# Kernel tuning notes

Measured on AMD Instinct MI355X. Metric: run time of the kernel, lower is better.

The kernel has to match this reference:

```python
import jax, jax.numpy as jnp
import numpy as np

H, D = 20, 64  # heads, head_dim (hidden_size = 1280)


def setup_inputs() -> dict:
    key = jax.random.key(0)
    ks = jax.random.split(key, 10)
    B, S, HID, CROSS, T_TXT, T_IP = 8, 4096, 1280, 2048, 77, 4
    w = lambda k, shp: jax.random.normal(k, shp, dtype=jnp.float32) * 0.02
    return {
        "hidden_states": jax.random.normal(ks[0], (B, S, HID), dtype=jnp.float32),
        "encoder_hidden_states": jax.random.normal(ks[1], (B, T_TXT, CROSS), dtype=jnp.float32),
        "ip_hidden_states": jax.random.normal(ks[2], (B, T_IP, CROSS), dtype=jnp.float32),
        "Wq": w(ks[3], (HID, HID)),
        "Wk": w(ks[4], (CROSS, HID)),
        "Wv": w(ks[5], (CROSS, HID)),
        "Wk_ip": w(ks[6], (CROSS, HID)),
        "Wv_ip": w(ks[7], (CROSS, HID)),
        "Wo": w(ks[8], (HID, HID)),
        "bo": jnp.zeros((HID,), dtype=jnp.float32),
    }


def _attend(q, kv_in, Wk, Wv):
    # q: [B,S,H,D]; kv_in: [B,T,cross]
    B, T = kv_in.shape[0], kv_in.shape[1]
    k = (kv_in @ Wk).reshape(B, T, H, D)
    v = (kv_in @ Wv).reshape(B, T, H, D)
    scale = 1.0 / jnp.sqrt(jnp.asarray(D, q.dtype))
    scores = jnp.einsum("bqhd,bkhd->bhqk", q, k) * scale
    probs = jax.nn.softmax(scores, axis=-1)
    out = jnp.einsum("bhqk,bkhd->bqhd", probs, v)
    return out.reshape(B, q.shape[1], H * D)


def reference(hidden_states, encoder_hidden_states, ip_hidden_states,
              Wq, Wk, Wv, Wk_ip, Wv_ip, Wo, bo):
    B, S, _ = hidden_states.shape
    q = (hidden_states @ Wq).reshape(B, S, H, D)
    # text cross-attention branch
    out = _attend(q, encoder_hidden_states, Wk, Wv)
    # IP-adapter branch (single adapter, scale=1.0, no mask)
    ip_scale = 1.0
    out = out + ip_scale * _attend(q, ip_hidden_states, Wk_ip, Wv_ip)
    # output projection (dropout is identity at inference)
    return out @ Wo + bo
```

## Files before the change

kernel.cpp:

```cpp
#include <hip/hip_runtime.h>

using u16 = unsigned short;
using u32 = unsigned int;
typedef __bf16 bf16x8 __attribute__((ext_vector_type(8)));
typedef float f32x4 __attribute__((ext_vector_type(4)));
typedef float f32x16 __attribute__((ext_vector_type(16)));

__device__ __forceinline__ u16 f2bf(float f) {
  u32 u = __float_as_uint(f);
  u += 0x7FFFu + ((u >> 16) & 1u);
  return (u16)(u >> 16);
}

__device__ __forceinline__ u32 cvtpk(float a, float b) {
  u32 r;
  asm("v_cvt_pk_bf16_f32 %0, %1, %2" : "=v"(r) : "v"(a), "v"(b));
  return r;
}

__device__ __forceinline__ void gload16(const u16* g, u16* l) {
  __builtin_amdgcn_global_load_lds((const __attribute__((address_space(1))) void*)g,
                                   (__attribute__((address_space(3))) void*)l, 16, 0, 0);
}

__global__ void build_a_all(const float* __restrict__ enc, const float* __restrict__ ip,
                            u16* __restrict__ out) {
  const int i = blockIdx.x * 256 + threadIdx.x;
  const int row = i >> 9;
  const int c4 = i & 511;
  ushort4 o = {0, 0, 0, 0};
  const float4* src = nullptr;
  if (row < 616) src = (const float4*)enc + (size_t)row * 512 + c4;
  else if (row >= 640 && row < 672) src = (const float4*)ip + (size_t)(row - 640) * 512 + c4;
  if (src) {
    const float4 v = *src;
    o.x = f2bf(v.x); o.y = f2bf(v.y); o.z = f2bf(v.z); o.w = f2bf(v.w);
  }
  ((ushort4*)out)[i] = o;
}

__global__ void transpose_w4(const float* __restrict__ s0, const float* __restrict__ s1,
                             const float* __restrict__ s2, const float* __restrict__ s3,
                             u16* __restrict__ dst) {
  __shared__ float tile[32][33];
  const int z = blockIdx.z;
  const float* in = (z == 0) ? s0 : (z == 1) ? s1 : (z == 2) ? s2 : s3;
  u16* out = dst + (size_t)z * 1280 * 2048;
  const int K = 2048, N = 1280;
  const int n0 = blockIdx.x << 5, k0 = blockIdx.y << 5;
  const int x = threadIdx.x, y = threadIdx.y;
#pragma unroll
  for (int i = 0; i < 32; i += 8)
    tile[y + i][x] = in[(size_t)(k0 + y + i) * N + n0 + x];
  __syncthreads();
#pragma unroll
  for (int i = 0; i < 32; i += 8)
    out[(size_t)(n0 + y + i) * K + k0 + x] = f2bf(tile[x][y + i]);
}

__global__ void transpose_w2(const float* __restrict__ s0, const float* __restrict__ s1,
                             u16* __restrict__ d0, u16* __restrict__ d1) {
  __shared__ float tile[32][33];
  const int z = blockIdx.z;
  const float* in = z ? s1 : s0;
  u16* out = z ? d1 : d0;
  const int K = 1280, N = 1280;
  const int n0 = blockIdx.x << 5, k0 = blockIdx.y << 5;
  const int x = threadIdx.x, y = threadIdx.y;
#pragma unroll
  for (int i = 0; i < 32; i += 8)
    tile[y + i][x] = in[(size_t)(k0 + y + i) * N + n0 + x];
  __syncthreads();
#pragma unroll
  for (int i = 0; i < 32; i += 8)
    out[(size_t)(n0 + y + i) * K + k0 + x] = f2bf(tile[x][y + i]);
}

#define MFMA16(a, b, c) __builtin_amdgcn_mfma_f32_16x16x32_bf16(a, b, c, 0, 0, 0)
#define MFMA32(a, b, c) __builtin_amdgcn_mfma_f32_32x32x16_bf16(a, b, c, 0, 0, 0)

template <int MODE, int CONV>
__global__ __launch_bounds__(512, 2) void gemm256(
    const u16* __restrict__ A, const u16* __restrict__ Bt,
    u16* __restrict__ Cb, float* __restrict__ Cf, const float* __restrict__ bias,
    const u16* __restrict__ kvcP, const u16* __restrict__ vtP,
    const float* __restrict__ convSrc, u16* __restrict__ convDst,
    int M, int N, int K) {
  const int tid = threadIdx.x;

  if (CONV) {
    if (blockIdx.x >= 60) {
      const float4* src = (const float4*)convSrc;
      ushort4* dst = (ushort4*)convDst;
      const long base = (long)(blockIdx.x - 60) * 4096 + tid;
#pragma unroll
      for (int k = 0; k < 8; ++k) {
        const float4 v = src[base + k * 512];
        ushort4 o;
        o.x = f2bf(v.x); o.y = f2bf(v.y); o.z = f2bf(v.z); o.w = f2bf(v.w);
        dst[base + k * 512] = o;
      }
      return;
    }
  }

  __shared__ __align__(16) u16 smem[67584];
  u16* As = smem;
  u16* Bs = smem + 32768;

  const int w = tid >> 6, lane = tid & 63;
  const int lo = lane & 15, hi = lane >> 4;
  const int wm = w >> 2, wn = w & 3;

  const int nbn = N >> 8;
  int wg = blockIdx.x;
  if (!CONV) {
    const int nwg = gridDim.x;
    const int q = nwg >> 3, r = nwg & 7;
    const int xcd = wg & 7, l = wg >> 3;
    wg = (xcd < r ? xcd * (q + 1) : r * (q + 1) + (xcd - r) * q) + l;
  }
  const int bm = wg / nbn, bn = wg % nbn;
  const int m0 = bm << 8, n0 = bn << 8;
  const int NT = K >> 6;

  const int sr = lane >> 3;
  const int sc8 = ((lane & 7) ^ sr) << 3;
  const u16* pA[2];
  const u16* pB[2];
#pragma unroll
  for (int i = 0; i < 2; ++i) {
    const int rr = (i * 8 + w) * 8 + sr;
    pA[i] = A + (size_t)(m0 + rr) * K + sc8;
    pB[i] = Bt + (size_t)(n0 + rr) * K + sc8;
  }
  const int ch0 = w * 512, ch1 = (8 + w) * 512;

#define STAGE_A(h, tt)                                                     \
  {                                                                        \
    const int ttc = ((tt) < NT) ? (tt) : (NT - 1);                         \
    u16* d = As + ((((tt)&1) * 2 + (h)) << 13);                            \
    const size_t off = (size_t)(h)*128 * K + (size_t)ttc * 64;             \
    gload16(pA[0] + off, d + ch0);                                         \
    gload16(pA[1] + off, d + ch1);                                         \
  }
#define STAGE_B(h, tt)                                                     \
  {                                                                        \
    const int ttc = ((tt) < NT) ? (tt) : (NT - 1);                         \
    u16* d = Bs + ((((tt)&1) * 2 + (h)) << 13);                            \
    const size_t off = (size_t)(h)*128 * K + (size_t)ttc * 64;             \
    gload16(pB[0] + off, d + ch0);                                         \
    gload16(pB[1] + off, d + ch1);                                         \
  }

  const int low0 = (lo << 7) | ((hi ^ (lo & 7)) << 4);
  const int low1 = (lo << 7) | (((4 | hi) ^ (lo & 7)) << 4);

  f32x4 acc[8][4];
#pragma unroll
  for (int i = 0; i < 8; ++i)
#pragma unroll
    for (int j = 0; j < 4; ++j) acc[i][j] = (f32x4){0.f, 0.f, 0.f, 0.f};

  STAGE_B(0, 0); STAGE_B(1, 0);
  STAGE_A(0, 0); STAGE_A(1, 0);
  STAGE_B(0, 1); STAGE_B(1, 1);

  const char* aSm = (const char*)As;
  const char* bSm = (const char*)Bs;

  for (int t = 0; t < NT; ++t) {
    const int p = t & 1;
    const int aBase = (p * 2 + wm) << 14;
    const int bBase = ((p * 2 + (wn >> 1)) << 14) + ((wn & 1) << 13);

    asm volatile("s_waitcnt vmcnt(4)" ::: "memory");
    asm volatile("s_barrier" ::: "memory");

    bf16x8 a0[4][2], a1[4][2], b0[2][2], b1[2][2];
#pragma unroll
    for (int mf = 0; mf < 4; ++mf) {
      a0[mf][0] = *(const bf16x8*)(aSm + aBase + (mf << 11) + low0);
      a0[mf][1] = *(const bf16x8*)(aSm + aBase + (mf << 11) + low1);
    }
#pragma unroll
    for (int nf = 0; nf < 2; ++nf) {
      b0[nf][0] = *(const bf16x8*)(bSm + bBase + (nf << 11) + low0);
      b0[nf][1] = *(const bf16x8*)(bSm + bBase + (nf << 11) + low1);
    }
    STAGE_A(0, t + 1);
    __builtin_amdgcn_s_setprio(1);
#pragma unroll
    for (int mf = 0; mf < 4; ++mf)
#pragma unroll
      for (int nf = 0; nf < 2; ++nf) {
        acc[mf][nf] = MFMA16(a0[mf][0], b0[nf][0], acc[mf][nf]);
        acc[mf][nf] = MFMA16(a0[mf][1], b0[nf][1], acc[mf][nf]);
      }
    __builtin_amdgcn_s_setprio(0);

#pragma unroll
    for (int nf = 0; nf < 2; ++nf) {
      b1[nf][0] = *(const bf16x8*)(bSm + bBase + (1 << 12) + (nf << 11) + low0);
      b1[nf][1] = *(const bf16x8*)(bSm + bBase + (1 << 12) + (nf << 11) + low1);
    }
    STAGE_A(1, t + 1);
    __builtin_amdgcn_s_setprio(1);
#pragma unroll
    for (int mf = 0; mf < 4; ++mf)
#pragma unroll
      for (int nf = 0; nf < 2; ++nf) {
        acc[mf][2 + nf] = MFMA16(a0[mf][0], b1[nf][0], acc[mf][2 + nf]);
        acc[mf][2 + nf] = MFMA16(a0[mf][1], b1[nf][1], acc[mf][2 + nf]);
      }
    __builtin_amdgcn_s_setprio(0);
    asm volatile("s_barrier" ::: "memory");

#pragma unroll
    for (int mf = 0; mf < 4; ++mf) {
      a1[mf][0] = *(const bf16x8*)(aSm + aBase + (1 << 13) + (mf << 11) + low0);
      a1[mf][1] = *(const bf16x8*)(aSm + aBase + (1 << 13) + (mf << 11) + low1);
    }
    STAGE_B(0, t + 2);
    __builtin_amdgcn_s_setprio(1);
#pragma unroll
    for (int mf = 0; mf < 4; ++mf)
#pragma unroll
      for (int nf = 0; nf < 2; ++nf) {
        acc[4 + mf][nf] = MFMA16(a1[mf][0], b0[nf][0], acc[4 + mf][nf]);
        acc[4 + mf][nf] = MFMA16(a1[mf][1], b0[nf][1], acc[4 + mf][nf]);
      }
    __builtin_amdgcn_s_setprio(0);

    STAGE_B(1, t + 2);
    __builtin_amdgcn_s_setprio(1);
#pragma unroll
    for (int mf = 0; mf < 4; ++mf)
#pragma unroll
      for (int nf = 0; nf < 2; ++nf) {
        acc[4 + mf][2 + nf] = MFMA16(a1[mf][0], b1[nf][0], acc[4 + mf][2 + nf]);
        acc[4 + mf][2 + nf] = MFMA16(a1[mf][1], b1[nf][1], acc[4 + mf][2 + nf]);
      }
    __builtin_amdgcn_s_setprio(0);
  }

  if (MODE != 2) {
#pragma unroll
    for (int g = 0; g < 2; ++g)
#pragma unroll
      for (int mf = 0; mf < 4; ++mf)
#pragma unroll
        for (int ng = 0; ng < 2; ++ng)
#pragma unroll
          for (int nfi = 0; nfi < 2; ++nfi) {
            const f32x4 v = acc[g * 4 + mf][ng * 2 + nfi];
            const int row0 = m0 + wm * 128 + g * 64 + mf * 16 + hi * 4;
            const int col = n0 + wn * 64 + ng * 32 + nfi * 16 + lo;
            if (MODE == 1) {
              const float bb = bias[col];
#pragma unroll
              for (int r = 0; r < 4; ++r)
                Cf[(size_t)(row0 + r) * N + col] = v[r] + bb;
            } else {
#pragma unroll
              for (int r = 0; r < 4; ++r)
                Cb[(size_t)(row0 + r) * N + col] = f2bf(v[r]);
            }
          }
  } else {
    const int l31 = lane & 31, hi5 = lane >> 5;
    const int h = bn * 4 + wn;
    const int b = m0 >> 12;

    bf16x8 kreg[3][4];
#pragma unroll
    for (int kf = 0; kf < 3; ++kf) {
      const int key = kf * 32 + l31;
      const u16* kp;
      if (key < 77) kp = kvcP + (size_t)(b * 77 + key) * 5120 + h * 64 + hi5 * 8;
      else if (key >= 80 && key < 84)
        kp = kvcP + (size_t)(640 + b * 4 + key - 80) * 5120 + 2560 + h * 64 + hi5 * 8;
      else kp = kvcP + h * 64 + hi5 * 8;
#pragma unroll
      for (int dc = 0; dc < 4; ++dc) kreg[kf][dc] = *(const bf16x8*)(kp + dc * 16);
    }

    asm volatile("s_waitcnt vmcnt(0)" ::: "memory");
    __builtin_amdgcn_s_barrier();

    u16* qlds = smem + w * 8448;
#pragma unroll
    for (int g = 0; g < 2; ++g)
#pragma unroll
      for (int mf = 0; mf < 4; ++mf)
#pragma unroll
        for (int ng = 0; ng < 2; ++ng)
#pragma unroll
          for (int nfi = 0; nfi < 2; ++nfi) {
            const f32x4 v = acc[g * 4 + mf][ng * 2 + nfi];
            const int qrow = g * 64 + mf * 16 + hi * 4;
            const int d = ng * 32 + nfi * 16 + lo;
#pragma unroll
            for (int r = 0; r < 4; ++r) qlds[(qrow + r) * 66 + d] = f2bf(v[r]);
          }

    const u16* vbase = vtP + ((size_t)(b * 20 + h) * 64) * 96 + hi5 * 8;
    const int rowB = m0 + wm * 128;

#pragma unroll
    for (int pass = 0; pass < 2; ++pass) {
      bf16x8 qf0[4], qf1[4];
#pragma unroll
      for (int dc = 0; dc < 4; ++dc) {
        qf0[dc] = *(const bf16x8*)&qlds[(pass * 64 + l31) * 66 + dc * 16 + hi5 * 8];
        qf1[dc] = *(const bf16x8*)&qlds[(pass * 64 + 32 + l31) * 66 + dc * 16 + hi5 * 8];
      }

      f32x16 s0[3], s1[3];
#pragma unroll
      for (int kf = 0; kf < 3; ++kf)
#pragma unroll
        for (int r = 0; r < 16; ++r) { s0[kf][r] = 0.f; s1[kf][r] = 0.f; }

#pragma unroll
      for (int kf = 0; kf < 3; ++kf)
#pragma unroll
        for (int dc = 0; dc < 4; ++dc) {
          s0[kf] = MFMA32(kreg[kf][dc], qf0[dc], s0[kf]);
          s1[kf] = MFMA32(kreg[kf][dc], qf1[dc], s1[kf]);
        }

      float st0 = 0.f, si0 = 0.f, st1 = 0.f, si1 = 0.f;
#pragma unroll
      for (int kf = 0; kf < 3; ++kf)
#pragma unroll
        for (int r = 0; r < 16; ++r) {
          const int krem = (r & 3) + 8 * (r >> 2);
          const int k = kf * 32 + krem + 4 * hi5;
          const bool vtx = k < 77;
          const bool vip = (k >= 80) & (k < 84);
          const float e0 = (vtx | vip) ? __expf(s0[kf][r] * 0.125f) : 0.f;
          const float e1 = (vtx | vip) ? __expf(s1[kf][r] * 0.125f) : 0.f;
          s0[kf][r] = e0; s1[kf][r] = e1;
          st0 += vtx ? e0 : 0.f; si0 += vip ? e0 : 0.f;
          st1 += vtx ? e1 : 0.f; si1 += vip ? e1 : 0.f;
        }
      st0 += __shfl_xor(st0, 32); si0 += __shfl_xor(si0, 32);
      st1 += __shfl_xor(st1, 32); si1 += __shfl_xor(si1, 32);
      const float rt0 = __fdividef(1.f, st0), ri0 = __fdividef(1.f, si0);
      const float rt1 = __fdividef(1.f, st1), ri1 = __fdividef(1.f, si1);
#pragma unroll
      for (int kf = 0; kf < 3; ++kf)
#pragma unroll
        for (int r = 0; r < 16; ++r) {
          const int krem = (r & 3) + 8 * (r >> 2);
          const int k = kf * 32 + krem + 4 * hi5;
          const bool vip = (k >= 80) & (k < 84);
          s0[kf][r] *= vip ? ri0 : rt0;
          s1[kf][r] *= vip ? ri1 : rt1;
        }

#define PV_STORE(sA, qoff)                                                  \
      {                                                                     \
        f32x16 pacc[2];                                                     \
        _Pragma("unroll") for (int nf = 0; nf < 2; ++nf)                    \
        _Pragma("unroll") for (int r = 0; r < 16; ++r) pacc[nf][r] = 0.f;   \
        _Pragma("unroll") for (int ks = 0; ks < 6; ++ks) {                  \
          const int kf = ks >> 1;                                           \
          const int rb = (ks & 1) * 8;                                      \
          const u32 lo01 = cvtpk(sA[kf][rb + 0], sA[kf][rb + 1]);           \
          const u32 lo23 = cvtpk(sA[kf][rb + 2], sA[kf][rb + 3]);           \
          const u32 hi01 = cvtpk(sA[kf][rb + 4], sA[kf][rb + 5]);           \
          const u32 hi23 = cvtpk(sA[kf][rb + 6], sA[kf][rb + 7]);           \
          const u32 plo01 = __shfl_xor(lo01, 32);                           \
          const u32 plo23 = __shfl_xor(lo23, 32);                           \
          const u32 phi01 = __shfl_xor(hi01, 32);                           \
          const u32 phi23 = __shfl_xor(hi23, 32);                           \
          union { u32 u[4]; bf16x8 v; } pu;                                 \
          pu.u[0] = hi5 ? phi01 : lo01;                                     \
          pu.u[1] = hi5 ? phi23 : lo23;                                     \
          pu.u[2] = hi5 ? hi01 : plo01;                                     \
          pu.u[3] = hi5 ? hi23 : plo23;                                     \
          _Pragma("unroll") for (int nf = 0; nf < 2; ++nf) {                \
            const bf16x8 vb = *(const bf16x8*)(vbase +                      \
                (size_t)(nf * 32 + l31) * 96 + ks * 16);                    \
            pacc[nf] = MFMA32(pu.v, vb, pacc[nf]);                          \
          }                                                                 \
        }                                                                   \
        _Pragma("unroll") for (int nf = 0; nf < 2; ++nf)                    \
        _Pragma("unroll") for (int r = 0; r < 16; ++r) {                    \
          const int row = rowB + pass * 64 + (qoff) +                       \
                          (r & 3) + 8 * (r >> 2) + 4 * hi5;                 \
          Cb[(size_t)row * 1280 + h * 64 + nf * 32 + l31] =                 \
              f2bf(pacc[nf][r]);                                            \
        }                                                                   \
      }

      PV_STORE(s0, 0)
      PV_STORE(s1, 32)
#undef PV_STORE
    }
  }
#undef STAGE_A
#undef STAGE_B
}

__global__ __launch_bounds__(256) void build_vt(const u16* __restrict__ kvc,
                                                u16* __restrict__ vt) {
  __shared__ u16 Ls[96][72];
  const int tid = threadIdx.x;
  const int h = blockIdx.x % 20, b = blockIdx.x / 20;
  for (int idx = tid; idx < 96 * 8; idx += 256) {
    const int row = idx >> 3, c8 = (idx & 7) << 3;
    uint4 val = make_uint4(0, 0, 0, 0);
    if (row < 77)
      val = *(const uint4*)(kvc + (size_t)(b * 77 + row) * 5120 + 1280 + h * 64 + c8);
    else if (row >= 80 && row < 84)
      val = *(const uint4*)(kvc + (size_t)(640 + b * 4 + row - 80) * 5120 + 3840 + h * 64 + c8);
    *(uint4*)&Ls[row][c8] = val;
  }
  __syncthreads();
  u16* dst = vt + (size_t)blockIdx.x * 64 * 96;
  for (int idx = tid; idx < 768; idx += 256) {
    const int d = idx / 12, c = (idx % 12) * 8;
    u16 tmp[8];
#pragma unroll
    for (int j = 0; j < 8; ++j) tmp[j] = Ls[c + j][d];
    *(uint4*)(dst + d * 96 + c) = *(const uint4*)tmp;
  }
}

extern "C" void kernel_launch(void* const* d_in, const int* in_sizes, int n_in,
                              void* d_out, int out_size, void* d_ws, size_t ws_size,
                              hipStream_t stream) {
  (void)in_sizes; (void)n_in; (void)out_size; (void)ws_size;
  const float* hs   = (const float*)d_in[0];
  const float* enc  = (const float*)d_in[1];
  const float* ip   = (const float*)d_in[2];
  const float* Wq   = (const float*)d_in[3];
  const float* Wk   = (const float*)d_in[4];
  const float* Wv   = (const float*)d_in[5];
  const float* Wkip = (const float*)d_in[6];
  const float* Wvip = (const float*)d_in[7];
  const float* Wo   = (const float*)d_in[8];
  const float* bo   = (const float*)d_in[9];
  float* out = (float*)d_out;

  u16* wq_t  = (u16*)d_out;
  u16* hs_bf = (u16*)d_out + 41943040;

  char* ws = (char*)d_ws;
  u16* kvc   = (u16*)(ws);
  u16* wo_t  = (u16*)(ws + 15728640);
  u16* vt    = (u16*)(ws + 19005440);
  u16* attn  = (u16*)(ws + 20971520);
  u16* kvw   = (u16*)(ws + 20971520 + 3276800);
  u16* a_all = (u16*)(ws + 20971520 + 24248320);

  build_a_all<<<1536, 256, 0, stream>>>(enc, ip, a_all);

  dim3 tb(32, 8);
  transpose_w4<<<dim3(40, 64, 4), tb, 0, stream>>>(Wk, Wv, Wkip, Wvip, kvw);
  transpose_w2<<<dim3(40, 40, 2), tb, 0, stream>>>(Wq, Wo, wq_t, wo_t);

  gemm256<0, 1><<<2620, 512, 0, stream>>>(a_all, kvw, kvc, nullptr, nullptr,
                                          nullptr, nullptr, hs, hs_bf,
                                          768, 5120, 2048);
  build_vt<<<160, 256, 0, stream>>>(kvc, vt);

  gemm256<2, 0><<<640, 512, 0, stream>>>(hs_bf, wq_t, attn, nullptr, nullptr,
                                         kvc, vt, nullptr, nullptr,
                                         32768, 1280, 1280);

  gemm256<1, 0><<<640, 512, 0, stream>>>(attn, wo_t, nullptr, out, bo,
                                         nullptr, nullptr, nullptr, nullptr,
                                         32768, 1280, 1280);
}
```

Before: 344.8 us.

## Merge prep kernels into one launch and use 128x128 tile GEMM for output projection

Folds the activation conversion and the two weight-transpose kernels into a single flattened launch to cut launch overhead. Replaces the 256-tile output projection GEMM with a new 128x128-tile, 256-thread kernel that uses double-buffered direct-to-LDS loads and XCD-aware block remapping. With 2560 blocks instead of 640, the output projection should balance better across CUs, at the cost of less data reuse per tile.

After: 334.9 us (median of 2 runs). -2.9%, faster.

```diff
diff --git a/kernel.cpp b/kernel.cpp
--- a/kernel.cpp
+++ b/kernel.cpp
@@ -23,32 +23,50 @@
                                    (__attribute__((address_space(3))) void*)l, 16, 0, 0);
 }
 
-__global__ void build_a_all(const float* __restrict__ enc, const float* __restrict__ ip,
-                            u16* __restrict__ out) {
-  const int i = blockIdx.x * 256 + threadIdx.x;
-  const int row = i >> 9;
-  const int c4 = i & 511;
-  ushort4 o = {0, 0, 0, 0};
-  const float4* src = nullptr;
-  if (row < 616) src = (const float4*)enc + (size_t)row * 512 + c4;
-  else if (row >= 640 && row < 672) src = (const float4*)ip + (size_t)(row - 640) * 512 + c4;
-  if (src) {
-    const float4 v = *src;
-    o.x = f2bf(v.x); o.y = f2bf(v.y); o.z = f2bf(v.z); o.w = f2bf(v.w);
-  }
-  ((ushort4*)out)[i] = o;
-}
-
-__global__ void transpose_w4(const float* __restrict__ s0, const float* __restrict__ s1,
-                             const float* __restrict__ s2, const float* __restrict__ s3,
-                             u16* __restrict__ dst) {
+__global__ void prep_all(const float* __restrict__ enc, const float* __restrict__ ip,
+                         u16* __restrict__ a_all,
+                         const float* __restrict__ Wk, const float* __restrict__ Wv,
+                         const float* __restrict__ Wkip, const float* __restrict__ Wvip,
+                         u16* __restrict__ kvw,
+                         const float* __restrict__ Wq, const float* __restrict__ Wo,
+                         u16* __restrict__ wq_t, u16* __restrict__ wo_t) {
+  const int bid = blockIdx.x;
+  const int tid = threadIdx.x;
+  if (bid < 1536) {
+    const int i = bid * 256 + tid;
+    const int row = i >> 9;
+    const int c4 = i & 511;
+    ushort4 o = {0, 0, 0, 0};
+    const float4* src = nullptr;
+    if (row < 616) src = (const float4*)enc + (size_t)row * 512 + c4;
+    else if (row >= 640 && row < 672) src = (const float4*)ip + (size_t)(row - 640) * 512 + c4;
+    if (src) {
+      const float4 v = *src;
+      o.x = f2bf(v.x); o.y = f2bf(v.y); o.z = f2bf(v.z); o.w = f2bf(v.w);
+    }
+    ((ushort4*)a_all)[i] = o;
+    return;
+  }
   __shared__ float tile[32][33];
-  const int z = blockIdx.z;
-  const float* in = (z == 0) ? s0 : (z == 1) ? s1 : (z == 2) ? s2 : s3;
-  u16* out = dst + (size_t)z * 1280 * 2048;
-  const int K = 2048, N = 1280;
-  const int n0 = blockIdx.x << 5, k0 = blockIdx.y << 5;
-  const int x = threadIdx.x, y = threadIdx.y;
+  const int x = tid & 31, y = tid >> 5;
+  const float* in;
+  u16* out;
+  int K, N, n0, k0;
+  if (bid < 11776) {
+    const int f = bid - 1536;
+    const int z = f / 2560, rem = f % 2560;
+    in = (z == 0) ? Wk : (z == 1) ? Wv : (z == 2) ? Wkip : Wvip;
+    out = kvw + (size_t)z * 1280 * 2048;
+    K = 2048; N = 1280;
+    n0 = (rem % 40) << 5; k0 = (rem / 40) << 5;
+  } else {
+    const int f = bid - 11776;
+    const int z = f / 1600, rem = f % 1600;
+    in = z ? Wo : Wq;
+    out = z ? wo_t : wq_t;
+    K = 1280; N = 1280;
+    n0 = (rem % 40) << 5; k0 = (rem / 40) << 5;
+  }
 #pragma unroll
   for (int i = 0; i < 32; i += 8)
     tile[y + i][x] = in[(size_t)(k0 + y + i) * N + n0 + x];
@@ -58,32 +76,13 @@
     out[(size_t)(n0 + y + i) * K + k0 + x] = f2bf(tile[x][y + i]);
 }
 
-__global__ void transpose_w2(const float* __restrict__ s0, const float* __restrict__ s1,
-                             u16* __restrict__ d0, u16* __restrict__ d1) {
-  __shared__ float tile[32][33];
-  const int z = blockIdx.z;
-  const float* in = z ? s1 : s0;
-  u16* out = z ? d1 : d0;
-  const int K = 1280, N = 1280;
-  const int n0 = blockIdx.x << 5, k0 = blockIdx.y << 5;
-  const int x = threadIdx.x, y = threadIdx.y;
-#pragma unroll
-  for (int i = 0; i < 32; i += 8)
-    tile[y + i][x] = in[(size_t)(k0 + y + i) * N + n0 + x];
-  __syncthreads();
-#pragma unroll
-  for (int i = 0; i < 32; i += 8)
-    out[(size_t)(n0 + y + i) * K + k0 + x] = f2bf(tile[x][y + i]);
-}
-
 #define MFMA16(a, b, c) __builtin_amdgcn_mfma_f32_16x16x32_bf16(a, b, c, 0, 0, 0)
 #define MFMA32(a, b, c) __builtin_amdgcn_mfma_f32_32x32x16_bf16(a, b, c, 0, 0, 0)
 
 template <int MODE, int CONV>
 __global__ __launch_bounds__(512, 2) void gemm256(
     const u16* __restrict__ A, const u16* __restrict__ Bt,
-    u16* __restrict__ Cb, float* __restrict__ Cf, const float* __restrict__ bias,
-    const u16* __restrict__ kvcP, const u16* __restrict__ vtP,
+    u16* __restrict__ Cb, const u16* __restrict__ kvcP, const u16* __restrict__ vtP,
     const float* __restrict__ convSrc, u16* __restrict__ convDst,
     int M, int N, int K) {
   const int tid = threadIdx.x;
@@ -256,16 +255,9 @@
             const f32x4 v = acc[g * 4 + mf][ng * 2 + nfi];
             const int row0 = m0 + wm * 128 + g * 64 + mf * 16 + hi * 4;
             const int col = n0 + wn * 64 + ng * 32 + nfi * 16 + lo;
-            if (MODE == 1) {
-              const float bb = bias[col];
-#pragma unroll
-              for (int r = 0; r < 4; ++r)
-                Cf[(size_t)(row0 + r) * N + col] = v[r] + bb;
-            } else {
-#pragma unroll
-              for (int r = 0; r < 4; ++r)
-                Cb[(size_t)(row0 + r) * N + col] = f2bf(v[r]);
-            }
+#pragma unroll
+            for (int r = 0; r < 4; ++r)
+              Cb[(size_t)(row0 + r) * N + col] = f2bf(v[r]);
           }
   } else {
     const int l31 = lane & 31, hi5 = lane >> 5;
@@ -405,6 +397,109 @@
 #undef STAGE_B
 }
 
+__global__ __launch_bounds__(256, 2) void gemm128(
+    const u16* __restrict__ A, const u16* __restrict__ Bt,
+    float* __restrict__ Cf, const float* __restrict__ bias,
+    int M, int N, int K) {
+  __shared__ __align__(16) u16 smem[32768];
+  const int tid = threadIdx.x;
+  const int w = tid >> 6, lane = tid & 63;
+  const int lo = lane & 15, hi = lane >> 4;
+  const int wm = w >> 1, wn = w & 1;
+
+  const int nbn = N >> 7;
+  int wg = blockIdx.x;
+  {
+    const int nwg = gridDim.x;
+    const int q = nwg >> 3, r = nwg & 7;
+    const int xcd = wg & 7, l = wg >> 3;
+    wg = (xcd < r ? xcd * (q + 1) : r * (q + 1) + (xcd - r) * q) + l;
+  }
+  const int bm = wg / nbn, bn = wg % nbn;
+  const int m0 = bm << 7, n0 = bn << 7;
+  const int NT = K >> 6;
+
+  const int sr = lane >> 3;
+  const int sc8 = ((lane & 7) ^ sr) << 3;
+  const u16 *pA[4], *pB[4];
+#pragma unroll
+  for (int j = 0; j < 4; ++j) {
+    const int rr = (w + j * 4) * 8 + sr;
+    pA[j] = A + (size_t)(m0 + rr) * K + sc8;
+    pB[j] = Bt + (size_t)(n0 + rr) * K + sc8;
+  }
+
+#define STG128(tt)                                                         \
+  {                                                                        \
+    const int ttc = ((tt) < NT) ? (tt) : (NT - 1);                         \
+    const int bofs = (((tt)&1) << 13);          \
+    const size_t off = (size_t)ttc * 64;                                   \
+    _Pragma("unroll") for (int j = 0; j < 4; ++j) {                        \
+      gload16(pA[j] + off, smem + bofs + (w + j * 4) * 512);               \
+      gload16(pB[j] + off, smem + 16384 + bofs + (w + j * 4) * 512);       \
+    }                                                                      \
+  }
+
+  const int low0 = (lo << 7) | ((hi ^ (lo & 7)) << 4);
+  const int low1 = (lo << 7) | (((4 | hi) ^ (lo & 7)) << 4);
+  const char* aSm = (const char*)smem;
+  const char* bSm = (const char*)(smem + 16384);
+
+  f32x4 acc[4][4];
+#pragma unroll
+  for (int i = 0; i < 4; ++i)
+#pragma unroll
+    for (int j = 0; j < 4; ++j) acc[i][j] = (f32x4){0.f, 0.f, 0.f, 0.f};
+
+  STG128(0); STG128(1);
+
+  for (int t = 0; t < NT; ++t) {
+    const int aBase = ((t & 1) << 14) + (wm << 13);
+    const int bBase = ((t & 1) << 14) + (wn << 13);
+
+    asm volatile("s_waitcnt vmcnt(8)" ::: "memory");
+    asm volatile("s_barrier" ::: "memory");
+
+    bf16x8 a[4][2], b[4][2];
+#pragma unroll
+    for (int mf = 0; mf < 4; ++mf) {
+      a[mf][0] = *(const bf16x8*)(aSm + aBase + (mf << 11) + low0);
+      a[mf][1] = *(const bf16x8*)(aSm + aBase + (mf << 11) + low1);
+    }
+#pragma unroll
+    for (int nf = 0; nf < 4; ++nf) {
+      b[nf][0] = *(const bf16x8*)(bSm + bBase + (nf << 11) + low0);
+      b[nf][1] = *(const bf16x8*)(bSm + bBase + (nf << 11) + low1);
+    }
+    asm volatile("s_waitcnt lgkmcnt(0)" ::: "memory");
+    __builtin_amdgcn_sched_barrier(0);
+    asm volatile("s_barrier" ::: "memory");
+    STG128(t + 2);
+    __builtin_amdgcn_s_setprio(1);
+#pragma unroll
+    for (int mf = 0; mf < 4; ++mf)
+#pragma unroll
+      for (int nf = 0; nf < 4; ++nf) {
+        acc[mf][nf] = MFMA16(a[mf][0], b[nf][0], acc[mf][nf]);
+        acc[mf][nf] = MFMA16(a[mf][1], b[nf][1], acc[mf][nf]);
+      }
+    __builtin_amdgcn_s_setprio(0);
+  }
+
+#pragma unroll
+  for (int mf = 0; mf < 4; ++mf)
+#pragma unroll
+    for (int nf = 0; nf < 4; ++nf) {
+      const int row0 = m0 + wm * 64 + mf * 16 + hi * 4;
+      const int col = n0 + wn * 64 + nf * 16 + lo;
+      const float bb = bias[col];
+#pragma unroll
+      for (int r = 0; r < 4; ++r)
+        Cf[(size_t)(row0 + r) * N + col] = acc[mf][nf][r] + bb;
+    }
+#undef STG128
+}
+
 __global__ __launch_bounds__(256) void build_vt(const u16* __restrict__ kvc,
                                                 u16* __restrict__ vt) {
   __shared__ u16 Ls[96][72];
@@ -457,22 +552,15 @@
   u16* kvw   = (u16*)(ws + 20971520 + 3276800);
   u16* a_all = (u16*)(ws + 20971520 + 24248320);
 
-  build_a_all<<<1536, 256, 0, stream>>>(enc, ip, a_all);
-
-  dim3 tb(32, 8);
-  transpose_w4<<<dim3(40, 64, 4), tb, 0, stream>>>(Wk, Wv, Wkip, Wvip, kvw);
-  transpose_w2<<<dim3(40, 40, 2), tb, 0, stream>>>(Wq, Wo, wq_t, wo_t);
+  prep_all<<<14976, 256, 0, stream>>>(enc, ip, a_all, Wk, Wv, Wkip, Wvip, kvw,
+                                      Wq, Wo, wq_t, wo_t);
 
   gemm256<0, 1><<<2620, 512, 0, stream>>>(a_all, kvw, kvc, nullptr, nullptr,
-                                          nullptr, nullptr, hs, hs_bf,
-                                          768, 5120, 2048);
+                                          hs, hs_bf, 768, 5120, 2048);
   build_vt<<<160, 256, 0, stream>>>(kvc, vt);
 
-  gemm256<2, 0><<<640, 512, 0, stream>>>(hs_bf, wq_t, attn, nullptr, nullptr,
-                                         kvc, vt, nullptr, nullptr,
-                                         32768, 1280, 1280);
-
-  gemm256<1, 0><<<640, 512, 0, stream>>>(attn, wo_t, nullptr, out, bo,
-                                         nullptr, nullptr, nullptr, nullptr,
-                                         32768, 1280, 1280);
-}
+  gemm256<2, 0><<<640, 512, 0, stream>>>(hs_bf, wq_t, attn, kvc, vt,
+                                         nullptr, nullptr, 32768, 1280, 1280);
+
+  gemm128<<<2560, 256, 0, stream>>>(attn, wo_t, out, bo, 32768, 1280, 1280);
+}
```
